# Performance work log

Measured on AMD Instinct MI355X. Metric: run time of the kernel, lower is better.

## Reference

```python
import jax, jax.numpy as jnp
import numpy as np


def setup_inputs() -> dict:
    key = jax.random.key(0)
    ks = jax.random.split(key, 10)
    B, C, H = 128, 768, 12
    d = C // H
    t_h = t_w = 8
    s_h = s_w = 16
    Nt = t_h * t_w * 2          # 128 template tokens
    Ns = s_h * s_w + 4          # 260 search tokens
    N = Nt + Ns                 # 388
    s = 0.02
    return {
        "x": jax.random.normal(ks[0], (B, N, C), jnp.float32),
        "mem": jax.random.normal(ks[1], (B, H, d, d), jnp.float32),
        "z": jnp.ones((B, H, d, 1), jnp.float32),
        "qkv_w": jax.random.normal(ks[2], (3 * C, C), jnp.float32) * s,
        "qkv_b": jnp.zeros((3 * C,), jnp.float32),
        "proj_w": jax.random.normal(ks[3], (C, C), jnp.float32) * s,
        "proj_b": jnp.zeros((C,), jnp.float32),
        "memk_w": jax.random.normal(ks[4], (C, C), jnp.float32) * s,
        "memk_b": jnp.zeros((C,), jnp.float32),
        "memv_w": jax.random.normal(ks[5], (C, C), jnp.float32) * s,
        "memv_b": jnp.zeros((C,), jnp.float32),
        "betas": jax.random.normal(ks[6], (1, H, 1, d), jnp.float32),
        "t_h": t_h, "t_w": t_w, "s_h": s_h, "s_w": s_w,
    }


def reference(x, mem, z, qkv_w, qkv_b, proj_w, proj_b,
              memk_w, memk_b, memv_w, memv_b, betas,
              t_h, t_w, s_h, s_w):
    B, N, C = x.shape
    H = betas.shape[1]
    d = C // H
    Nt = t_h * t_w * 2
    Ns = s_h * s_w + 4
    scale = 1.0 / jnp.sqrt(jnp.float32(d))

    qkv = x @ qkv_w.T + qkv_b                       # [B,N,3C]
    qkv = qkv.reshape(B, N, 3, C)
    q_f, k_f, v_f = qkv[:, :, 0], qkv[:, :, 1], qkv[:, :, 2]  # [B,N,C]

    def heads(t):  # [B,N,C] -> [B,H,N,d]
        return t.reshape(B, -1, H, d).transpose(0, 2, 1, 3)

    q, k, v = heads(q_f), heads(k_f), heads(v_f)

    # memory k/v projections act on the raw (C-dim) search split of k,v
    k_s_mem = heads(k_f[:, Nt:, :] @ memk_w.T + memk_b)  # [B,H,Ns,d]
    v_s_mem = heads(v_f[:, Nt:, :] @ memv_w.T + memv_b)  # [B,H,Ns,d]

    q_mt, q_s = q[:, :, :Nt], q[:, :, Nt:]
    k_mt = k[:, :, :Nt]
    v_mt = v[:, :, :Nt]

    # template self-attention (q_mt only attends to k_mt)
    attn_mt = jax.nn.softmax(jnp.einsum('bhqd,bhkd->bhqk', q_mt, k_mt) * scale, axis=-1)
    x_mt = jnp.einsum('bhqk,bhkd->bhqd', attn_mt, v_mt)          # [B,H,Nt,d]
    x_mt = x_mt.transpose(0, 2, 1, 3).reshape(B, Nt, C)

    # search attends to full sequence
    attn_s = jax.nn.softmax(jnp.einsum('bhqd,bhkd->bhqk', q_s, k) * scale, axis=-1)
    x_s = jnp.einsum('bhqk,bhkd->bhqd', attn_s, v)               # [B,H,Ns,d]

    # linear-attention memory read (ELU feature map)
    sigma_q = jax.nn.elu(q_s) + 1.0                              # [B,H,Ns,d]
    att_mem = (sigma_q @ mem) / (sigma_q @ z)                    # [B,H,Ns,d]

    # delta-rule memory update
    sigma_k = jax.nn.elu(k_s_mem) + 1.0                          # [B,H,Ns,d]
    zz = jnp.sum(sigma_k, axis=-2, keepdims=True).swapaxes(-2, -1)  # [B,H,d,1]
    pred = (sigma_k @ mem) / (sigma_k @ z)                       # [B,H,Ns,d]
    mem_new = mem + jnp.einsum('bhnd,bhne->bhde', sigma_k, v_s_mem - pred)
    z_new = z + zz

    beta = jax.nn.sigmoid(betas)                                 # [1,H,1,d]
    x_s = beta * att_mem + (1.0 - beta) * x_s
    x_s = x_s.transpose(0, 2, 1, 3).reshape(B, Ns, C)

    out = jnp.concatenate([x_mt, x_s], axis=1) @ proj_w.T + proj_b
    return out, mem_new, z_new
```

## Files before the change

### kernel.cpp

```cpp
#include <hip/hip_runtime.h>

typedef unsigned short u16;
typedef __attribute__((ext_vector_type(8))) short  vbf8;
typedef __attribute__((ext_vector_type(4))) float  vf4;

#define B_   128
#define N_   388
#define NT   128
#define NS   260
#define C_   768
#define H_   12
#define D_   64
#define K3   2304

#define QKV_LEN  114425856ll
#define KSM_LEN  25559040ll
#define CAT_LEN  38141952ll
#define MEM_LEN  6291456ll

#define SPS  288
#define SPL  296

#define WOFF_QKV  0ll
#define WOFF_MEMK 1769472ll
#define WOFF_MEMV 2359296ll
#define WOFF_PROJ 2949120ll
#define WTOT     3538944ll
__device__ __align__(16) u16 g_wbf[3538944];

__device__ __forceinline__ float bf2f(u16 u) {
    union { unsigned int i; float f; } v; v.i = ((unsigned int)u) << 16; return v.f;
}
__device__ __forceinline__ u16 f2bf(float f) {
    union { float f; unsigned int i; } v; v.f = f;
    unsigned int r = v.i + 0x7fffu + ((v.i >> 16) & 1u);
    return (u16)(r >> 16);
}
__device__ __forceinline__ float elu1(float x) { return x > 0.f ? x + 1.f : __expf(x); }

__device__ __forceinline__ void gload_lds16(const u16* g, u16* l) {
    __builtin_amdgcn_global_load_lds(
        (const __attribute__((address_space(1))) unsigned int*)g,
        (__attribute__((address_space(3))) unsigned int*)l, 16, 0, 0);
}

__global__ __launch_bounds__(256) void convert_bf16(
    const float* __restrict__ src, u16* __restrict__ dst, long long n)
{
    long long i0 = ((long long)blockIdx.x * 256 + threadIdx.x) * 8;
    long long stride = (long long)gridDim.x * 256 * 8;
    for (long long i = i0; i < n; i += stride) {
        float4 a = *(const float4*)(src + i);
        float4 b = *(const float4*)(src + i + 4);
        ushort4 u1; u1.x = f2bf(a.x); u1.y = f2bf(a.y); u1.z = f2bf(a.z); u1.w = f2bf(a.w);
        ushort4 u2; u2.x = f2bf(b.x); u2.y = f2bf(b.y); u2.z = f2bf(b.z); u2.w = f2bf(b.w);
        *(ushort4*)(dst + i)     = u1;
        *(ushort4*)(dst + i + 4) = u2;
    }
}

__global__ __launch_bounds__(256) void convert_wbf_all(
    const float* __restrict__ s0, const float* __restrict__ s1,
    const float* __restrict__ s2, const float* __restrict__ s3)
{
    long long i = ((long long)blockIdx.x * 256 + threadIdx.x) * 8;
    if (i >= WTOT) return;
    const float* src; long long off;
    if (i < WOFF_MEMK)      { src = s0; off = i; }
    else if (i < WOFF_MEMV) { src = s1; off = i - WOFF_MEMK; }
    else if (i < WOFF_PROJ) { src = s2; off = i - WOFF_MEMV; }
    else                    { src = s3; off = i - WOFF_PROJ; }
    float4 a = *(const float4*)(src + off);
    float4 b = *(const float4*)(src + off + 4);
    ushort4 u1; u1.x = f2bf(a.x); u1.y = f2bf(a.y); u1.z = f2bf(a.z); u1.w = f2bf(a.w);
    ushort4 u2; u2.x = f2bf(b.x); u2.y = f2bf(b.y); u2.z = f2bf(b.z); u2.w = f2bf(b.w);
    *(ushort4*)(g_wbf + i)     = u1;
    *(ushort4*)(g_wbf + i + 4) = u2;
}

__global__ __launch_bounds__(256) void memT_kernel(
    const float* __restrict__ memin, u16* __restrict__ memT)
{
    __shared__ float ml[64 * 65];
    int bh = blockIdx.x, t = threadIdx.x;
    const float* src = memin + (long long)bh * 4096;
#pragma unroll
    for (int i = 0; i < 16; i++) {
        int idx = i * 256 + t;
        ml[(idx >> 6) * 65 + (idx & 63)] = src[idx];
    }
    __syncthreads();
    u16* dst = memT + (long long)bh * 4096;
#pragma unroll
    for (int i = 0; i < 16; i++) {
        int o = i * 256 + t;
        int dout = o >> 6, din = o & 63;
        dst[o] = f2bf(ml[din * 65 + dout]);
    }
}

template<int CF32>
__global__ __launch_bounds__(256) void gemm_mfma(
    const u16* __restrict__ A, long long off0, int rows_per_b,
    long long stride_b, long long stride_r,
    long long w_off, const float* __restrict__ bias,
    void* __restrict__ Cv, int Nout, int nbx)
{
    __shared__ __align__(16) u16 lds[2][2][4096];

    const u16* W = g_wbf + w_off;
    int t = threadIdx.x;

    int wg = blockIdx.x;
    wg = (wg & 7) * ((int)gridDim.x >> 3) + (wg >> 3);
    int m0 = (wg / nbx) * 128;
    int n0 = (wg % nbx) * 128;

    int lane = t & 63, w = t >> 6;
    int w512 = w * 512;

    int srow  = t >> 2;
    int scol  = (((t & 3) ^ (srow & 3))) * 8;
    long long aoff0, aoff1;
    {
        int g1 = m0 + srow, g2 = g1 + 64;
        int b1 = g1 / rows_per_b, j1 = g1 - b1 * rows_per_b;
        int b2 = g2 / rows_per_b, j2 = g2 - b2 * rows_per_b;
        aoff0 = off0 + (long long)b1 * stride_b + (long long)j1 * stride_r + scol;
        aoff1 = off0 + (long long)b2 * stride_b + (long long)j2 * stride_r + scol;
    }
    const u16* wp0 = W + (long long)(n0 + srow) * 768 + scol;
    const u16* wp1 = W + (long long)(n0 + srow + 64) * 768 + scol;

    int lr = lane & 15, kg = lane >> 4;
    int wm = w >> 1, wn = w & 1;
    int aslot = (kg ^ (lr & 3)) * 8;
    int abase = (wm * 64 + lr) * 32 + aslot;
    int bbase = (wn * 64 + lr) * 32 + aslot;

    vf4 acc[4][4];
#pragma unroll
    for (int i = 0; i < 4; i++)
#pragma unroll
        for (int j = 0; j < 4; j++) acc[i][j] = vf4{0.f, 0.f, 0.f, 0.f};

    auto stage = [&](int buf, int kt) {
        gload_lds16(A + aoff0 + kt, &lds[buf][0][w512]);
        gload_lds16(A + aoff1 + kt, &lds[buf][0][2048 + w512]);
        gload_lds16(wp0 + kt,       &lds[buf][1][w512]);
        gload_lds16(wp1 + kt,       &lds[buf][1][2048 + w512]);
    };

    stage(0, 0);
    __syncthreads();

    int cur = 0;
    for (int kt = 0; kt < 768; kt += 32) {
        if (kt != 736) stage(cur ^ 1, kt + 32);

        vbf8 af[4], bf[4];
#pragma unroll
        for (int f = 0; f < 4; f++) {
            af[f] = *(const vbf8*)&lds[cur][0][abase + f * 512];
            bf[f] = *(const vbf8*)&lds[cur][1][bbase + f * 512];
        }
#pragma unroll
        for (int i = 0; i < 4; i++)
#pragma unroll
            for (int j = 0; j < 4; j++)
                acc[i][j] = __builtin_amdgcn_mfma_f32_16x16x32_bf16(
                    af[i], bf[j], acc[i][j], 0, 0, 0);

        __syncthreads();
        cur ^= 1;
    }

    if (!CF32) {
        u16* ct = &lds[0][0][0];
#pragma unroll
        for (int i = 0; i < 4; i++)
#pragma unroll
            for (int j = 0; j < 4; j++) {
                int col = wn * 64 + j * 16 + lr;
                float bb = bias[n0 + col];
#pragma unroll
                for (int r = 0; r < 4; r++)
                    ct[(wm * 64 + i * 16 + kg * 4 + r) * 128 + col] =
                        f2bf(acc[i][j][r] + bb);
            }
        __syncthreads();
        int col0 = (t & 15) * 8;
#pragma unroll
        for (int rr = 0; rr < 8; rr++) {
            int row_l = rr * 16 + (t >> 4);
            vbf8 v = *(const vbf8*)&ct[row_l * 128 + col0];
            *(vbf8*)((u16*)Cv + (long long)(m0 + row_l) * Nout + n0 + col0) = v;
        }
    } else {
        float* cf = (float*)&lds[0][0][0];
#pragma unroll
        for (int p = 0; p < 2; p++) {
            if (wm == p) {
#pragma unroll
                for (int i = 0; i < 4; i++)
#pragma unroll
                    for (int j = 0; j < 4; j++) {
                        int col = wn * 64 + j * 16 + lr;
                        float bb = bias[n0 + col];
#pragma unroll
                        for (int r = 0; r < 4; r++)
                            cf[(i * 16 + kg * 4 + r) * 128 + col] =
                                acc[i][j][r] + bb;
                    }
            }
            __syncthreads();
            int col0 = (t & 15) * 8;
#pragma unroll
            for (int rr = 0; rr < 4; rr++) {
                int row_l = rr * 16 + (t >> 4);
                float4 v0 = *(const float4*)&cf[row_l * 128 + col0];
                float4 v1 = *(const float4*)&cf[row_l * 128 + col0 + 4];
                float* dst = (float*)Cv + (long long)(m0 + p * 64 + row_l) * Nout + n0 + col0;
                *(float4*)dst = v0;
                *(float4*)(dst + 4) = v1;
            }
            __syncthreads();
        }
    }
}

#define SKP 416
#define VTS 424
__global__ __launch_bounds__(512) void attn_s_mfma(
    const u16* __restrict__ qkv, const u16* __restrict__ memT,
    const float* __restrict__ zin, const float* __restrict__ betas,
    u16* __restrict__ concat)
{
    __shared__ __align__(16) u16 Kl[SKP * 64];
    __shared__ __align__(16) u16 Vt[64 * VTS];
    __shared__ __align__(16) u16 Pl[8][16 * 40];
    __shared__ float red[8][16];

    int bh = blockIdx.x;
    int b = bh / H_, h = bh % H_;
    int t = threadIdx.x, lane = t & 63, w = t >> 6;
    int lr = lane & 15, q4 = lane >> 4;

    {
        int key0 = t >> 3;
        int d0 = (t & 7) * 8;
        for (int kp = 0; kp < SKP; kp += 64) {
            int key = kp + key0;
            if (key < SKP) {
                vbf8 kv, vv;
#pragma unroll
                for (int u = 0; u < 8; u++) { ((short*)&kv)[u] = 0; ((short*)&vv)[u] = 0; }
                if (key < N_) {
                    const u16* base = qkv + ((long long)(b * N_ + key)) * K3 + h * D_;
                    kv = *(const vbf8*)(base + C_ + d0);
                    vv = *(const vbf8*)(base + 2 * C_ + d0);
                }
                *(vbf8*)((char*)Kl + ((key * 128 + d0 * 2) ^ ((key & 7) << 4))) = kv;
#pragma unroll
                for (int u = 0; u < 8; u++) Vt[(d0 + u) * VTS + key] = ((u16*)&vv)[u];
            }
        }
    }
    __syncthreads();

    const float* zp = zin + bh * 64;
    const u16* mtb = memT + (long long)bh * 4096;

    for (int s = w; s < 17; s += 8) {
        int qtok = NT + s * 16 + lr;
        if (qtok > N_ - 1) qtok = N_ - 1;
        const u16* qbase = qkv + ((long long)(b * N_ + qtok)) * K3 + h * D_;
        vbf8 qf0 = *(const vbf8*)(qbase + q4 * 8);
        vbf8 qf1 = *(const vbf8*)(qbase + 32 + q4 * 8);

        vbf8 qs0, qs1;
#pragma unroll
        for (int j = 0; j < 8; j++) {
            ((u16*)&qs0)[j] = f2bf(bf2f(((u16*)&qf0)[j]) * 0.125f);
            ((u16*)&qs1)[j] = f2bf(bf2f(((u16*)&qf1)[j]) * 0.125f);
        }

        vf4 S[13][2];
#pragma unroll
        for (int kt = 0; kt < 13; kt++) {
#pragma unroll
            for (int ks = 0; ks < 2; ks++) {
                int krow = kt * 32 + ks * 16 + lr;
                int swz = (krow & 7) << 4;
                vbf8 b0 = *(const vbf8*)((char*)Kl + ((krow * 128 + q4 * 16) ^ swz));
                vbf8 b1 = *(const vbf8*)((char*)Kl + ((krow * 128 + 64 + q4 * 16) ^ swz));
                vf4 z4 = vf4{0.f, 0.f, 0.f, 0.f};
                vf4 sv = __builtin_amdgcn_mfma_f32_16x16x32_bf16(qs0, b0, z4, 0, 0, 0);
                S[kt][ks] = __builtin_amdgcn_mfma_f32_16x16x32_bf16(qs1, b1, sv, 0, 0, 0);
            }
        }
#pragma unroll
        for (int ks = 0; ks < 2; ks++)
#pragma unroll
            for (int r = 0; r < 4; r++)
                if (ks * 16 + lr >= 4) S[12][ks][r] = -1e30f;

        float mx[4];
#pragma unroll
        for (int r = 0; r < 4; r++) mx[r] = S[0][0][r];
#pragma unroll
        for (int kt = 0; kt < 13; kt++)
#pragma unroll
            for (int ks = 0; ks < 2; ks++)
#pragma unroll
                for (int r = 0; r < 4; r++) mx[r] = fmaxf(mx[r], S[kt][ks][r]);
#pragma unroll
        for (int off = 1; off <= 8; off <<= 1)
#pragma unroll
            for (int r = 0; r < 4; r++) mx[r] = fmaxf(mx[r], __shfl_xor(mx[r], off));

        float l[4] = {0.f, 0.f, 0.f, 0.f};
#pragma unroll
        for (int kt = 0; kt < 13; kt++)
#pragma unroll
            for (int ks = 0; ks < 2; ks++)
#pragma unroll
                for (int r = 0; r < 4; r++) {
                    float p = __expf(S[kt][ks][r] - mx[r]);
                    S[kt][ks][r] = p;
                    l[r] += p;
                }
#pragma unroll
        for (int off = 1; off <= 8; off <<= 1)
#pragma unroll
            for (int r = 0; r < 4; r++) l[r] += __shfl_xor(l[r], off);

        vf4 accO[4];
#pragma unroll
        for (int dc = 0; dc < 4; dc++) accO[dc] = vf4{0.f, 0.f, 0.f, 0.f};
#pragma unroll
        for (int kt = 0; kt < 13; kt++) {
            u16* pw = Pl[w];
#pragma unroll
            for (int ks = 0; ks < 2; ks++)
#pragma unroll
                for (int r = 0; r < 4; r++)
                    pw[(q4 * 4 + r) * 40 + ks * 16 + lr] = f2bf(S[kt][ks][r]);
            vbf8 pf = *(const vbf8*)&Pl[w][lr * 40 + q4 * 8];
#pragma unroll
            for (int dc = 0; dc < 4; dc++) {
                vbf8 vf_ = *(const vbf8*)&Vt[(dc * 16 + lr) * VTS + kt * 32 + q4 * 8];
                accO[dc] = __builtin_amdgcn_mfma_f32_16x16x32_bf16(pf, vf_, accO[dc], 0, 0, 0);
            }
        }

        float invl[4];
#pragma unroll
        for (int r = 0; r < 4; r++) invl[r] = 1.f / l[r];

        vbf8 sq0, sq1;
        float dpart = 0.f;
#pragma unroll
        for (int j = 0; j < 8; j++) {
            float s0 = elu1(bf2f(((u16*)&qf0)[j]));
            float s1 = elu1(bf2f(((u16*)&qf1)[j]));
            ((u16*)&sq0)[j] = f2bf(s0);
            ((u16*)&sq1)[j] = f2bf(s1);
            dpart += s0 * zp[q4 * 8 + j] + s1 * zp[32 + q4 * 8 + j];
        }
        dpart += __shfl_xor(dpart, 16);
        dpart += __shfl_xor(dpart, 32);
        if (q4 == 0) red[w][lr] = dpart;

        vf4 am[4];
#pragma unroll
        for (int dc = 0; dc < 4; dc++) {
            vbf8 b0 = *(const vbf8*)(mtb + (dc * 16 + lr) * 64 + q4 * 8);
            vbf8 b1 = *(const vbf8*)(mtb + (dc * 16 + lr) * 64 + 32 + q4 * 8);
            vf4 z4 = vf4{0.f, 0.f, 0.f, 0.f};
            vf4 a = __builtin_amdgcn_mfma_f32_16x16x32_bf16(sq0, b0, z4, 0, 0, 0);
            am[dc] = __builtin_amdgcn_mfma_f32_16x16x32_bf16(sq1, b1, a, 0, 0, 0);
        }
        float den[4];
#pragma unroll
        for (int r = 0; r < 4; r++) den[r] = 1.f / red[w][q4 * 4 + r];

#pragma unroll
        for (int dc = 0; dc < 4; dc++) {
            float bb = betas[h * D_ + dc * 16 + lr];
            float beta = 1.f / (1.f + __expf(-bb));
#pragma unroll
            for (int r = 0; r < 4; r++) {
                int qs = s * 16 + q4 * 4 + r;
                if (qs < NS) {
                    float o = beta * (am[dc][r] * den[r]) +
                              (1.f - beta) * (accO[dc][r] * invl[r]);
                    concat[((long long)(b * N_ + NT + qs)) * C_ + h * D_ + dc * 16 + lr] = f2bf(o);
                }
            }
        }
    }
}

#define MTS 136
__global__ __launch_bounds__(512) void attn_mt_mfma(
    const u16* __restrict__ qkv, u16* __restrict__ concat)
{
    __shared__ __align__(16) u16 Kl[NT * 64];
    __shared__ __align__(16) u16 Vt[64 * MTS];
    __shared__ __align__(16) u16 Pl[8][16 * 40];

    int bh = blockIdx.x;
    int b = bh / H_, h = bh % H_;
    int t = threadIdx.x, lane = t & 63, w = t >> 6;
    int lr = lane & 15, q4 = lane >> 4;

    {
        int key0 = t >> 3;
        int d0 = (t & 7) * 8;
#pragma unroll
        for (int kp = 0; kp < NT; kp += 64) {
            int key = kp + key0;
            const u16* base = qkv + ((long long)(b * N_ + key)) * K3 + h * D_;
            vbf8 kv = *(const vbf8*)(base + C_ + d0);
            vbf8 vv = *(const vbf8*)(base + 2 * C_ + d0);
            *(vbf8*)((char*)Kl + ((key * 128 + d0 * 2) ^ ((key & 7) << 4))) = kv;
#pragma unroll
            for (int u = 0; u < 8; u++) Vt[(d0 + u) * MTS + key] = ((u16*)&vv)[u];
        }
    }
    __syncthreads();

    int qtok = w * 16 + lr;
    const u16* qbase = qkv + ((long long)(b * N_ + qtok)) * K3 + h * D_;
    vbf8 qf0 = *(const vbf8*)(qbase + q4 * 8);
    vbf8 qf1 = *(const vbf8*)(qbase + 32 + q4 * 8);
    vbf8 qs0, qs1;
#pragma unroll
    for (int j = 0; j < 8; j++) {
        ((u16*)&qs0)[j] = f2bf(bf2f(((u16*)&qf0)[j]) * 0.125f);
        ((u16*)&qs1)[j] = f2bf(bf2f(((u16*)&qf1)[j]) * 0.125f);
    }

    vf4 S[4][2];
#pragma unroll
    for (int kt = 0; kt < 4; kt++) {
#pragma unroll
        for (int ks = 0; ks < 2; ks++) {
            int krow = kt * 32 + ks * 16 + lr;
            int swz = (krow & 7) << 4;
            vbf8 b0 = *(const vbf8*)((char*)Kl + ((krow * 128 + q4 * 16) ^ swz));
            vbf8 b1 = *(const vbf8*)((char*)Kl + ((krow * 128 + 64 + q4 * 16) ^ swz));
            vf4 z4 = vf4{0.f, 0.f, 0.f, 0.f};
            vf4 sv = __builtin_amdgcn_mfma_f32_16x16x32_bf16(qs0, b0, z4, 0, 0, 0);
            S[kt][ks] = __builtin_amdgcn_mfma_f32_16x16x32_bf16(qs1, b1, sv, 0, 0, 0);
        }
    }

    float mx[4];
#pragma unroll
    for (int r = 0; r < 4; r++) mx[r] = S[0][0][r];
#pragma unroll
    for (int kt = 0; kt < 4; kt++)
#pragma unroll
        for (int ks = 0; ks < 2; ks++)
#pragma unroll
            for (int r = 0; r < 4; r++) mx[r] = fmaxf(mx[r], S[kt][ks][r]);
#pragma unroll
    for (int off = 1; off <= 8; off <<= 1)
#pragma unroll
        for (int r = 0; r < 4; r++) mx[r] = fmaxf(mx[r], __shfl_xor(mx[r], off));

    float l[4] = {0.f, 0.f, 0.f, 0.f};
#pragma unroll
    for (int kt = 0; kt < 4; kt++)
#pragma unroll
        for (int ks = 0; ks < 2; ks++)
#pragma unroll
            for (int r = 0; r < 4; r++) {
                float p = __expf(S[kt][ks][r] - mx[r]);
                S[kt][ks][r] = p;
                l[r] += p;
            }
#pragma unroll
    for (int off = 1; off <= 8; off <<= 1)
#pragma unroll
        for (int r = 0; r < 4; r++) l[r] += __shfl_xor(l[r], off);

    vf4 accO[4];
#pragma unroll
    for (int dc = 0; dc < 4; dc++) accO[dc] = vf4{0.f, 0.f, 0.f, 0.f};
#pragma unroll
    for (int kt = 0; kt < 4; kt++) {
        u16* pw = Pl[w];
#pragma unroll
        for (int ks = 0; ks < 2; ks++)
#pragma unroll
            for (int r = 0; r < 4; r++)
                pw[(q4 * 4 + r) * 40 + ks * 16 + lr] = f2bf(S[kt][ks][r]);
        vbf8 pf = *(const vbf8*)&Pl[w][lr * 40 + q4 * 8];
#pragma unroll
        for (int dc = 0; dc < 4; dc++) {
            vbf8 vf_ = *(const vbf8*)&Vt[(dc * 16 + lr) * MTS + kt * 32 + q4 * 8];
            accO[dc] = __builtin_amdgcn_mfma_f32_16x16x32_bf16(pf, vf_, accO[dc], 0, 0, 0);
        }
    }

    float invl[4];
#pragma unroll
    for (int r = 0; r < 4; r++) invl[r] = 1.f / l[r];

    int qt0 = w * 16;
#pragma unroll
    for (int dc = 0; dc < 4; dc++)
#pragma unroll
        for (int r = 0; r < 4; r++) {
            int row = qt0 + q4 * 4 + r;
            concat[((long long)(b * N_ + row)) * C_ + h * D_ + dc * 16 + lr] =
                f2bf(accO[dc][r] * invl[r]);
        }
}

__global__ __launch_bounds__(512) void sigma_pred_mem(
    const u16* __restrict__ ksm, const u16* __restrict__ vsm,
    const u16* __restrict__ memT, const float* __restrict__ zin,
    const float* __restrict__ memin, float* __restrict__ mem_out,
    float* __restrict__ z_out)
{
    __shared__ __align__(16) u16 sigL[64][SPL];
    __shared__ __align__(16) u16 wL[64][SPL];
    __shared__ float red[8][16];
    __shared__ float zpart[8][64];
    __shared__ float zlds[64];

    int bh = blockIdx.x;
    int b = bh / H_, h = bh % H_;
    int t = threadIdx.x, lane = t & 63, w = t >> 6;
    int lr = lane & 15, q4 = lane >> 4;

    if (t < 64) zlds[t] = zin[bh * 64 + t];
    __syncthreads();

    const u16* mtb = memT + (long long)bh * 4096;
    float zacc[16];
#pragma unroll
    for (int j = 0; j < 16; j++) zacc[j] = 0.f;

    for (int s = w; s < 18; s += 8) {
        int n0 = s * 16;
        int nrow = n0 + lr;
        bool vrow = nrow < NS;
        int nclamp = vrow ? nrow : NS - 1;
        const u16* kbase = ksm + ((long long)(b * NS + nclamp)) * C_ + h * D_;
        vbf8 k0 = *(const vbf8*)(kbase + q4 * 8);
        vbf8 k1 = *(const vbf8*)(kbase + 32 + q4 * 8);

        vbf8 sq0, sq1;
        float dpart = 0.f;
#pragma unroll
        for (int j = 0; j < 8; j++) {
            float s0 = vrow ? elu1(bf2f(((u16*)&k0)[j])) : 0.f;
            float s1 = vrow ? elu1(bf2f(((u16*)&k1)[j])) : 0.f;
            u16 b0 = f2bf(s0), b1 = f2bf(s1);
            ((u16*)&sq0)[j] = b0;
            ((u16*)&sq1)[j] = b1;
            zacc[j]     += s0;
            zacc[8 + j] += s1;
            dpart += s0 * zlds[q4 * 8 + j] + s1 * zlds[32 + q4 * 8 + j];
            sigL[q4 * 8 + j][n0 + lr]      = b0;
            sigL[32 + q4 * 8 + j][n0 + lr] = b1;
        }
        dpart += __shfl_xor(dpart, 16);
        dpart += __shfl_xor(dpart, 32);
        if (q4 == 0) red[w][lr] = dpart;

        vf4 am[4];
#pragma unroll
        for (int dc = 0; dc < 4; dc++) {
            vbf8 b0 = *(const vbf8*)(mtb + (dc * 16 + lr) * 64 + q4 * 8);
            vbf8 b1 = *(const vbf8*)(mtb + (dc * 16 + lr) * 64 + 32 + q4 * 8);
            vf4 z4 = vf4{0.f, 0.f, 0.f, 0.f};
            vf4 a = __builtin_amdgcn_mfma_f32_16x16x32_bf16(sq0, b0, z4, 0, 0, 0);
            am[dc] = __builtin_amdgcn_mfma_f32_16x16x32_bf16(sq1, b1, a, 0, 0, 0);
        }
        float rden[4];
#pragma unroll
        for (int r = 0; r < 4; r++) rden[r] = 1.f / red[w][q4 * 4 + r];

#pragma unroll
        for (int dc = 0; dc < 4; dc++) {
            int e = dc * 16 + lr;
#pragma unroll
            for (int r = 0; r < 4; r++) {
                int nn = n0 + q4 * 4 + r;
                float wv = 0.f;
                if (nn < NS) {
                    float pv = am[dc][r] * rden[r];
                    wv = bf2f(vsm[((long long)(b * NS + nn)) * C_ + h * D_ + e]) - pv;
                }
                wL[e][n0 + q4 * 4 + r] = f2bf(wv);
            }
        }
    }

#pragma unroll
    for (int off = 1; off <= 8; off <<= 1)
#pragma unroll
        for (int j = 0; j < 16; j++) zacc[j] += __shfl_xor(zacc[j], off);
    if (lr == 0) {
#pragma unroll
        for (int j = 0; j < 8; j++) {
            zpart[w][q4 * 8 + j]      = zacc[j];
            zpart[w][32 + q4 * 8 + j] = zacc[8 + j];
        }
    }
    __syncthreads();

    if (t < 64) {
        float tot = 0.f;
#pragma unroll
        for (int ww = 0; ww < 8; ww++) tot += zpart[ww][t];
        z_out[bh * 64 + t] = zlds[t] + tot;
    }

    long long mb = (long long)bh * 4096;
#pragma unroll
    for (int p = 0; p < 2; p++) {
        int tid2 = w * 2 + p;
        int i = tid2 >> 2, j = tid2 & 3;
        vf4 acc = vf4{0.f, 0.f, 0.f, 0.f};
#pragma unroll
        for (int kt = 0; kt < SPS; kt += 32) {
            vbf8 af = *(const vbf8*)&sigL[i * 16 + lr][kt + q4 * 8];
            vbf8 bf = *(const vbf8*)&wL[j * 16 + lr][kt + q4 * 8];
            acc = __builtin_amdgcn_mfma_f32_16x16x32_bf16(af, bf, acc, 0, 0, 0);
        }
        int e = j * 16 + lr;
#pragma unroll
        for (int r = 0; r < 4; r++) {
            int dd = i * 16 + q4 * 4 + r;
            mem_out[mb + dd * 64 + e] = memin[mb + dd * 64 + e] + acc[r];
        }
    }
}

extern "C" void kernel_launch(void* const* d_in, const int* in_sizes, int n_in,
                              void* d_out, int out_size, void* d_ws, size_t ws_size,
                              hipStream_t stream)
{
    const float* x      = (const float*)d_in[0];
    const float* mem    = (const float*)d_in[1];
    const float* z      = (const float*)d_in[2];
    const float* qkv_w  = (const float*)d_in[3];
    const float* qkv_b  = (const float*)d_in[4];
    const float* proj_w = (const float*)d_in[5];
    const float* proj_b = (const float*)d_in[6];
    const float* memk_w = (const float*)d_in[7];
    const float* memk_b = (const float*)d_in[8];
    const float* memv_w = (const float*)d_in[9];
    const float* memv_b = (const float*)d_in[10];
    const float* betas  = (const float*)d_in[11];

    u16* ws     = (u16*)d_ws;
    u16* qkv    = ws;
    u16* ksm    = qkv + QKV_LEN;
    u16* vsm    = ksm + KSM_LEN;
    u16* concat = vsm + KSM_LEN;

    float* out     = (float*)d_out;
    float* mem_out = out + CAT_LEN;
    float* z_out   = mem_out + MEM_LEN;

    u16* x_bf = concat;
    u16* memT = (u16*)out;

    convert_bf16<<<dim3(2048), dim3(256), 0, stream>>>(x, x_bf, CAT_LEN);
    convert_wbf_all<<<dim3(1728), dim3(256), 0, stream>>>(qkv_w, memk_w, memv_w, proj_w);
    memT_kernel<<<dim3(B_ * H_), dim3(256), 0, stream>>>(mem, memT);

    gemm_mfma<0><<<dim3(6984), dim3(256), 0, stream>>>(
        x_bf, 0ll, 49664, 0ll, 768ll, WOFF_QKV, qkv_b, qkv, K3, 18);
    gemm_mfma<0><<<dim3(1560), dim3(256), 0, stream>>>(
        qkv, (long long)(NT * K3 + C_), NS, (long long)N_ * K3, (long long)K3,
        WOFF_MEMK, memk_b, ksm, C_, 6);
    gemm_mfma<0><<<dim3(1560), dim3(256), 0, stream>>>(
        qkv, (long long)(NT * K3 + 2 * C_), NS, (long long)N_ * K3, (long long)K3,
        WOFF_MEMV, memv_b, vsm, C_, 6);
    attn_s_mfma<<<dim3(B_ * H_), dim3(512), 0, stream>>>(
        qkv, memT, z, betas, concat);
    attn_mt_mfma<<<dim3(B_ * H_), dim3(512), 0, stream>>>(qkv, concat);
    sigma_pred_mem<<<dim3(B_ * H_), dim3(512), 0, stream>>>(
        ksm, vsm, memT, z, mem, mem_out, z_out);
    gemm_mfma<1><<<dim3(2328), dim3(256), 0, stream>>>(
        concat, 0ll, 49664, 0ll, 768ll, WOFF_PROJ, proj_b, out, C_, 6);
}
```

Measured before the change: 887.3 us.

## Fuse conversion kernels, dual memk/memv GEMM launch, and merge template attention into search kernel

Merges the x and weight bf16 conversions into one launch and runs the memk and memv projections as a single grid with two halves. Folds template self-attention into the search-attention kernel so the K/V already staged in LDS (the first 128 keys) are reused instead of reloaded by a separate kernel. This removes launch gaps and duplicate K/V loads from global memory. In exchange the fused attention kernel does more work per block, with waves 1-7 handling the template queries after the search work, which lengthens the critical path of each block.

```diff
diff --git a/kernel.cpp b/kernel.cpp
--- a/kernel.cpp
+++ b/kernel.cpp
@@ -44,38 +44,38 @@
         (__attribute__((address_space(3))) unsigned int*)l, 16, 0, 0);
 }
 
-__global__ __launch_bounds__(256) void convert_bf16(
-    const float* __restrict__ src, u16* __restrict__ dst, long long n)
-{
-    long long i0 = ((long long)blockIdx.x * 256 + threadIdx.x) * 8;
-    long long stride = (long long)gridDim.x * 256 * 8;
-    for (long long i = i0; i < n; i += stride) {
-        float4 a = *(const float4*)(src + i);
-        float4 b = *(const float4*)(src + i + 4);
+__global__ __launch_bounds__(256) void convert_all(
+    const float* __restrict__ x, u16* __restrict__ x_bf,
+    const float* __restrict__ s0, const float* __restrict__ s1,
+    const float* __restrict__ s2, const float* __restrict__ s3)
+{
+    int bid = blockIdx.x;
+    if (bid < 2048) {
+        long long i0 = ((long long)bid * 256 + threadIdx.x) * 8;
+        long long stride = 2048ll * 256 * 8;
+        for (long long i = i0; i < CAT_LEN; i += stride) {
+            float4 a = *(const float4*)(x + i);
+            float4 b = *(const float4*)(x + i + 4);
+            ushort4 u1; u1.x = f2bf(a.x); u1.y = f2bf(a.y); u1.z = f2bf(a.z); u1.w = f2bf(a.w);
+            ushort4 u2; u2.x = f2bf(b.x); u2.y = f2bf(b.y); u2.z = f2bf(b.z); u2.w = f2bf(b.w);
+            *(ushort4*)(x_bf + i)     = u1;
+            *(ushort4*)(x_bf + i + 4) = u2;
+        }
+    } else {
+        long long i = ((long long)(bid - 2048) * 256 + threadIdx.x) * 8;
+        if (i >= WTOT) return;
+        const float* src; long long off;
+        if (i < WOFF_MEMK)      { src = s0; off = i; }
+        else if (i < WOFF_MEMV) { src = s1; off = i - WOFF_MEMK; }
+        else if (i < WOFF_PROJ) { src = s2; off = i - WOFF_MEMV; }
+        else                    { src = s3; off = i - WOFF_PROJ; }
+        float4 a = *(const float4*)(src + off);
+        float4 b = *(const float4*)(src + off + 4);
         ushort4 u1; u1.x = f2bf(a.x); u1.y = f2bf(a.y); u1.z = f2bf(a.z); u1.w = f2bf(a.w);
         ushort4 u2; u2.x = f2bf(b.x); u2.y = f2bf(b.y); u2.z = f2bf(b.z); u2.w = f2bf(b.w);
-        *(ushort4*)(dst + i)     = u1;
-        *(ushort4*)(dst + i + 4) = u2;
-    }
-}
-
-__global__ __launch_bounds__(256) void convert_wbf_all(
-    const float* __restrict__ s0, const float* __restrict__ s1,
-    const float* __restrict__ s2, const float* __restrict__ s3)
-{
-    long long i = ((long long)blockIdx.x * 256 + threadIdx.x) * 8;
-    if (i >= WTOT) return;
-    const float* src; long long off;
-    if (i < WOFF_MEMK)      { src = s0; off = i; }
-    else if (i < WOFF_MEMV) { src = s1; off = i - WOFF_MEMK; }
-    else if (i < WOFF_PROJ) { src = s2; off = i - WOFF_MEMV; }
-    else                    { src = s3; off = i - WOFF_PROJ; }
-    float4 a = *(const float4*)(src + off);
-    float4 b = *(const float4*)(src + off + 4);
-    ushort4 u1; u1.x = f2bf(a.x); u1.y = f2bf(a.y); u1.z = f2bf(a.z); u1.w = f2bf(a.w);
-    ushort4 u2; u2.x = f2bf(b.x); u2.y = f2bf(b.y); u2.z = f2bf(b.z); u2.w = f2bf(b.w);
-    *(ushort4*)(g_wbf + i)     = u1;
-    *(ushort4*)(g_wbf + i + 4) = u2;
+        *(ushort4*)(g_wbf + i)     = u1;
+        *(ushort4*)(g_wbf + i + 4) = u2;
+    }
 }
 
 __global__ __launch_bounds__(256) void memT_kernel(
@@ -100,19 +100,18 @@
 }
 
 template<int CF32>
-__global__ __launch_bounds__(256) void gemm_mfma(
+__device__ __forceinline__ void gemm_body(
+    int wgid, int ngrid,
     const u16* __restrict__ A, long long off0, int rows_per_b,
     long long stride_b, long long stride_r,
-    long long w_off, const float* __restrict__ bias,
+    const u16* __restrict__ W, const float* __restrict__ bias,
     void* __restrict__ Cv, int Nout, int nbx)
 {
     __shared__ __align__(16) u16 lds[2][2][4096];
 
-    const u16* W = g_wbf + w_off;
     int t = threadIdx.x;
 
-    int wg = blockIdx.x;
-    wg = (wg & 7) * ((int)gridDim.x >> 3) + (wg >> 3);
+    int wg = (wgid & 7) * (ngrid >> 3) + (wgid >> 3);
     int m0 = (wg / nbx) * 128;
     int n0 = (wg % nbx) * 128;
 
@@ -229,9 +228,36 @@
     }
 }
 
+template<int CF32>
+__global__ __launch_bounds__(256) void gemm_mfma(
+    const u16* __restrict__ A, long long off0, int rows_per_b,
+    long long stride_b, long long stride_r,
+    long long w_off, const float* __restrict__ bias,
+    void* __restrict__ Cv, int Nout, int nbx)
+{
+    gemm_body<CF32>(blockIdx.x, gridDim.x, A, off0, rows_per_b, stride_b,
+                    stride_r, g_wbf + w_off, bias, Cv, Nout, nbx);
+}
+
+__global__ __launch_bounds__(256) void gemm_mfma_dual(
+    const u16* __restrict__ A, long long off0a, long long off0b,
+    int rows_per_b, long long stride_b, long long stride_r,
+    long long w_offa, long long w_offb,
+    const float* __restrict__ biasa, const float* __restrict__ biasb,
+    void* __restrict__ Cva, void* __restrict__ Cvb, int Nout, int nbx, int half)
+{
+    int bid = blockIdx.x;
+    if (bid < half)
+        gemm_body<0>(bid, half, A, off0a, rows_per_b, stride_b, stride_r,
+                     g_wbf + w_offa, biasa, Cva, Nout, nbx);
+    else
+        gemm_body<0>(bid - half, half, A, off0b, rows_per_b, stride_b, stride_r,
+                     g_wbf + w_offb, biasb, Cvb, Nout, nbx);
+}
+
 #define SKP 416
 #define VTS 424
-__global__ __launch_bounds__(512) void attn_s_mfma(
+__global__ __launch_bounds__(512) void attn_fused(
     const u16* __restrict__ qkv, const u16* __restrict__ memT,
     const float* __restrict__ zin, const float* __restrict__ betas,
     u16* __restrict__ concat)
@@ -400,125 +426,99 @@
             }
         }
     }
-}
-
-#define MTS 136
-__global__ __launch_bounds__(512) void attn_mt_mfma(
-    const u16* __restrict__ qkv, u16* __restrict__ concat)
-{
-    __shared__ __align__(16) u16 Kl[NT * 64];
-    __shared__ __align__(16) u16 Vt[64 * MTS];
-    __shared__ __align__(16) u16 Pl[8][16 * 40];
-
-    int bh = blockIdx.x;
-    int b = bh / H_, h = bh % H_;
-    int t = threadIdx.x, lane = t & 63, w = t >> 6;
-    int lr = lane & 15, q4 = lane >> 4;
-
-    {
-        int key0 = t >> 3;
-        int d0 = (t & 7) * 8;
-#pragma unroll
-        for (int kp = 0; kp < NT; kp += 64) {
-            int key = kp + key0;
-            const u16* base = qkv + ((long long)(b * N_ + key)) * K3 + h * D_;
-            vbf8 kv = *(const vbf8*)(base + C_ + d0);
-            vbf8 vv = *(const vbf8*)(base + 2 * C_ + d0);
-            *(vbf8*)((char*)Kl + ((key * 128 + d0 * 2) ^ ((key & 7) << 4))) = kv;
-#pragma unroll
-            for (int u = 0; u < 8; u++) Vt[(d0 + u) * MTS + key] = ((u16*)&vv)[u];
-        }
-    }
-    __syncthreads();
-
-    int qtok = w * 16 + lr;
-    const u16* qbase = qkv + ((long long)(b * N_ + qtok)) * K3 + h * D_;
-    vbf8 qf0 = *(const vbf8*)(qbase + q4 * 8);
-    vbf8 qf1 = *(const vbf8*)(qbase + 32 + q4 * 8);
-    vbf8 qs0, qs1;
-#pragma unroll
-    for (int j = 0; j < 8; j++) {
-        ((u16*)&qs0)[j] = f2bf(bf2f(((u16*)&qf0)[j]) * 0.125f);
-        ((u16*)&qs1)[j] = f2bf(bf2f(((u16*)&qf1)[j]) * 0.125f);
-    }
-
-    vf4 S[4][2];
-#pragma unroll
-    for (int kt = 0; kt < 4; kt++) {
-#pragma unroll
-        for (int ks = 0; ks < 2; ks++) {
-            int krow = kt * 32 + ks * 16 + lr;
-            int swz = (krow & 7) << 4;
-            vbf8 b0 = *(const vbf8*)((char*)Kl + ((krow * 128 + q4 * 16) ^ swz));
-            vbf8 b1 = *(const vbf8*)((char*)Kl + ((krow * 128 + 64 + q4 * 16) ^ swz));
-            vf4 z4 = vf4{0.f, 0.f, 0.f, 0.f};
-            vf4 sv = __builtin_amdgcn_mfma_f32_16x16x32_bf16(qs0, b0, z4, 0, 0, 0);
-            S[kt][ks] = __builtin_amdgcn_mfma_f32_16x16x32_bf16(qs1, b1, sv, 0, 0, 0);
-        }
-    }
-
-    float mx[4];
-#pragma unroll
-    for (int r = 0; r < 4; r++) mx[r] = S[0][0][r];
-#pragma unroll
-    for (int kt = 0; kt < 4; kt++)
-#pragma unroll
-        for (int ks = 0; ks < 2; ks++)
-#pragma unroll
-            for (int r = 0; r < 4; r++) mx[r] = fmaxf(mx[r], S[kt][ks][r]);
-#pragma unroll
-    for (int off = 1; off <= 8; off <<= 1)
-#pragma unroll
-        for (int r = 0; r < 4; r++) mx[r] = fmaxf(mx[r], __shfl_xor(mx[r], off));
-
-    float l[4] = {0.f, 0.f, 0.f, 0.f};
-#pragma unroll
-    for (int kt = 0; kt < 4; kt++)
-#pragma unroll
-        for (int ks = 0; ks < 2; ks++)
-#pragma unroll
-            for (int r = 0; r < 4; r++) {
-                float p = __expf(S[kt][ks][r] - mx[r]);
-                S[kt][ks][r] = p;
-                l[r] += p;
-            }
-#pragma unroll
-    for (int off = 1; off <= 8; off <<= 1)
-#pragma unroll
-        for (int r = 0; r < 4; r++) l[r] += __shfl_xor(l[r], off);
-
-    vf4 accO[4];
-#pragma unroll
-    for (int dc = 0; dc < 4; dc++) accO[dc] = vf4{0.f, 0.f, 0.f, 0.f};
-#pragma unroll
-    for (int kt = 0; kt < 4; kt++) {
-        u16* pw = Pl[w];
-#pragma unroll
-        for (int ks = 0; ks < 2; ks++)
-#pragma unroll
-            for (int r = 0; r < 4; r++)
-                pw[(q4 * 4 + r) * 40 + ks * 16 + lr] = f2bf(S[kt][ks][r]);
-        vbf8 pf = *(const vbf8*)&Pl[w][lr * 40 + q4 * 8];
-#pragma unroll
-        for (int dc = 0; dc < 4; dc++) {
-            vbf8 vf_ = *(const vbf8*)&Vt[(dc * 16 + lr) * MTS + kt * 32 + q4 * 8];
-            accO[dc] = __builtin_amdgcn_mfma_f32_16x16x32_bf16(pf, vf_, accO[dc], 0, 0, 0);
-        }
-    }
-
-    float invl[4];
-#pragma unroll
-    for (int r = 0; r < 4; r++) invl[r] = 1.f / l[r];
-
-    int qt0 = w * 16;
-#pragma unroll
-    for (int dc = 0; dc < 4; dc++)
-#pragma unroll
-        for (int r = 0; r < 4; r++) {
-            int row = qt0 + q4 * 4 + r;
-            concat[((long long)(b * N_ + row)) * C_ + h * D_ + dc * 16 + lr] =
-                f2bf(accO[dc][r] * invl[r]);
-        }
+
+    if (w > 0) {
+        for (int m = w - 1; m < 8; m += 7) {
+            int qtok = m * 16 + lr;
+            const u16* qbase = qkv + ((long long)(b * N_ + qtok)) * K3 + h * D_;
+            vbf8 qf0 = *(const vbf8*)(qbase + q4 * 8);
+            vbf8 qf1 = *(const vbf8*)(qbase + 32 + q4 * 8);
+            vbf8 qs0, qs1;
+#pragma unroll
+            for (int j = 0; j < 8; j++) {
+                ((u16*)&qs0)[j] = f2bf(bf2f(((u16*)&qf0)[j]) * 0.125f);
+                ((u16*)&qs1)[j] = f2bf(bf2f(((u16*)&qf1)[j]) * 0.125f);
+            }
+
+            vf4 S4[4][2];
+#pragma unroll
+            for (int kt = 0; kt < 4; kt++) {
+#pragma unroll
+                for (int ks = 0; ks < 2; ks++) {
+                    int krow = kt * 32 + ks * 16 + lr;
+                    int swz = (krow & 7) << 4;
+                    vbf8 b0 = *(const vbf8*)((char*)Kl + ((krow * 128 + q4 * 16) ^ swz));
+                    vbf8 b1 = *(const vbf8*)((char*)Kl + ((krow * 128 + 64 + q4 * 16) ^ swz));
+                    vf4 z4 = vf4{0.f, 0.f, 0.f, 0.f};
+                    vf4 sv = __builtin_amdgcn_mfma_f32_16x16x32_bf16(qs0, b0, z4, 0, 0, 0);
+                    S4[kt][ks] = __builtin_amdgcn_mfma_f32_16x16x32_bf16(qs1, b1, sv, 0, 0, 0);
+                }
+            }
+
+            float mx[4];
+#pragma unroll
+            for (int r = 0; r < 4; r++) mx[r] = S4[0][0][r];
+#pragma unroll
+            for (int kt = 0; kt < 4; kt++)
+#pragma unroll
+                for (int ks = 0; ks < 2; ks++)
+#pragma unroll
+                    for (int r = 0; r < 4; r++) mx[r] = fmaxf(mx[r], S4[kt][ks][r]);
+#pragma unroll
+            for (int off = 1; off <= 8; off <<= 1)
+#pragma unroll
+                for (int r = 0; r < 4; r++) mx[r] = fmaxf(mx[r], __shfl_xor(mx[r], off));
+
+            float l[4] = {0.f, 0.f, 0.f, 0.f};
+#pragma unroll
+            for (int kt = 0; kt < 4; kt++)
+#pragma unroll
+                for (int ks = 0; ks < 2; ks++)
+#pragma unroll
+                    for (int r = 0; r < 4; r++) {
+                        float p = __expf(S4[kt][ks][r] - mx[r]);
+                        S4[kt][ks][r] = p;
+                        l[r] += p;
+                    }
+#pragma unroll
+            for (int off = 1; off <= 8; off <<= 1)
+#pragma unroll
+                for (int r = 0; r < 4; r++) l[r] += __shfl_xor(l[r], off);
+
+            vf4 accO[4];
+#pragma unroll
+            for (int dc = 0; dc < 4; dc++) accO[dc] = vf4{0.f, 0.f, 0.f, 0.f};
+#pragma unroll
+            for (int kt = 0; kt < 4; kt++) {
+                u16* pw = Pl[w];
+#pragma unroll
+                for (int ks = 0; ks < 2; ks++)
+#pragma unroll
+                    for (int r = 0; r < 4; r++)
+                        pw[(q4 * 4 + r) * 40 + ks * 16 + lr] = f2bf(S4[kt][ks][r]);
+                vbf8 pf = *(const vbf8*)&Pl[w][lr * 40 + q4 * 8];
+#pragma unroll
+                for (int dc = 0; dc < 4; dc++) {
+                    vbf8 vf_ = *(const vbf8*)&Vt[(dc * 16 + lr) * VTS + kt * 32 + q4 * 8];
+                    accO[dc] = __builtin_amdgcn_mfma_f32_16x16x32_bf16(pf, vf_, accO[dc], 0, 0, 0);
+                }
+            }
+
+            float invl[4];
+#pragma unroll
+            for (int r = 0; r < 4; r++) invl[r] = 1.f / l[r];
+
+            int qt0 = m * 16;
+#pragma unroll
+            for (int dc = 0; dc < 4; dc++)
+#pragma unroll
+                for (int r = 0; r < 4; r++) {
+                    int row = qt0 + q4 * 4 + r;
+                    concat[((long long)(b * N_ + row)) * C_ + h * D_ + dc * 16 + lr] =
+                        f2bf(accO[dc][r] * invl[r]);
+                }
+        }
+    }
 }
 
 __global__ __launch_bounds__(512) void sigma_pred_mem(
@@ -674,21 +674,18 @@
     u16* x_bf = concat;
     u16* memT = (u16*)out;
 
-    convert_bf16<<<dim3(2048), dim3(256), 0, stream>>>(x, x_bf, CAT_LEN);
-    convert_wbf_all<<<dim3(1728), dim3(256), 0, stream>>>(qkv_w, memk_w, memv_w, proj_w);
+    convert_all<<<dim3(2048 + 1728), dim3(256), 0, stream>>>(
+        x, x_bf, qkv_w, memk_w, memv_w, proj_w);
     memT_kernel<<<dim3(B_ * H_), dim3(256), 0, stream>>>(mem, memT);
 
     gemm_mfma<0><<<dim3(6984), dim3(256), 0, stream>>>(
         x_bf, 0ll, 49664, 0ll, 768ll, WOFF_QKV, qkv_b, qkv, K3, 18);
-    gemm_mfma<0><<<dim3(1560), dim3(256), 0, stream>>>(
-        qkv, (long long)(NT * K3 + C_), NS, (long long)N_ * K3, (long long)K3,
-        WOFF_MEMK, memk_b, ksm, C_, 6);
-    gemm_mfma<0><<<dim3(1560), dim3(256), 0, stream>>>(
-        qkv, (long long)(NT * K3 + 2 * C_), NS, (long long)N_ * K3, (long long)K3,
-        WOFF_MEMV, memv_b, vsm, C_, 6);
-    attn_s_mfma<<<dim3(B_ * H_), dim3(512), 0, stream>>>(
+    gemm_mfma_dual<<<dim3(3120), dim3(256), 0, stream>>>(
+        qkv, (long long)(NT * K3 + C_), (long long)(NT * K3 + 2 * C_),
+        NS, (long long)N_ * K3, (long long)K3,
+        WOFF_MEMK, WOFF_MEMV, memk_b, memv_b, ksm, vsm, C_, 6, 1560);
+    attn_fused<<<dim3(B_ * H_), dim3(512), 0, stream>>>(
         qkv, memT, z, betas, concat);
-    attn_mt_mfma<<<dim3(B_ * H_), dim3(512), 0, stream>>>(qkv, concat);
     sigma_pred_mem<<<dim3(B_ * H_), dim3(512), 0, stream>>>(
         ksm, vsm, memT, z, mem, mem_out, z_out);
     gemm_mfma<1><<<dim3(2328), dim3(256), 0, stream>>>(
```

New measurement: 858.4 us. 3.3% less time.
